# Kernel tuning notes

Measured on AMD Instinct MI355X. Metric: run time of the kernel, lower is better.

## Reference

```python
import jax, jax.numpy as jnp
import numpy as np
import math


def setup_inputs() -> dict:
    key = jax.random.key(0)
    ks = jax.random.split(key, 5)
    B, L, H = 16384, 336, 168
    T = L + H
    T_air = jax.random.normal(ks[0], (B, T), dtype=jnp.float32) * 8.0 + 10.0
    T_obs = T_air + jax.random.normal(ks[1], (B, T), dtype=jnp.float32) * 2.0
    wind = jax.random.uniform(ks[2], (B, T), dtype=jnp.float32) * 10.0
    par = jax.random.uniform(ks[3], (B, T), dtype=jnp.float32) * 500.0
    dt = jax.random.uniform(ks[4], (B, T), dtype=jnp.float32) * 3600.0 + 1800.0
    k_init = 1e-4
    k_raw = jnp.float32(k_init + math.log(-math.expm1(-k_init)))  # softplus inverse
    return {
        "T_obs": T_obs, "T_air": T_air, "wind": wind, "par": par, "dt": dt,
        "L_hist": L,
        "k_raw": k_raw,
        "log_q": jnp.float32(-8.0), "log_r": jnp.float32(-4.0),
        "log_p0": jnp.float32(-2.0), "log_q_scale": jnp.float32(0.0),
        "theta_par_lin": jnp.float32(1e-5), "theta_par_quad": jnp.float32(1e-8),
        "theta_wind_cool": jnp.float32(-1e-5), "theta_sensible": jnp.float32(-1e-6),
        "theta_forced_conv": jnp.float32(-1e-7),
    }


def reference(T_obs, T_air, wind, par, dt, L_hist, k_raw, log_q, log_r, log_p0,
              log_q_scale, theta_par_lin, theta_par_quad, theta_wind_cool,
              theta_sensible, theta_forced_conv):
    B, T_total = T_obs.shape
    L = int(L_hist)
    H = T_total - L

    k = jax.nn.softplus(k_raw)
    q = jnp.exp(log_q)
    q_scale = jnp.exp(log_q_scale)
    R = jnp.exp(log_r)
    P0 = jnp.exp(log_p0)

    def predict(T, P, Ta, w, p, dtt):
        dT = T - Ta
        cl = (theta_par_lin * p + theta_par_quad * p * p + theta_wind_cool * w
              + theta_sensible * dT + theta_forced_conv * w * dT)
        T_pred = jnp.clip(T - k * dT * dtt + cl * dtt, -50.0, 100.0)
        F = jnp.clip(1.0 - k * dtt + (theta_sensible + theta_forced_conv * w) * dtt, -2.0, 2.0)
        P_pred = jnp.clip(F * F * P + q_scale * q * dtt, 1e-10, 1e6)
        return T_pred, P_pred

    def filt_step(carry, xs):
        T, P = carry
        Ta, w, p, dtt, y = xs
        Tp, Pp = predict(T, P, Ta, w, p, dtt)
        S = Pp + R
        K = Pp / S
        T_upd = Tp + K * (y - Tp)
        P_upd = (1.0 - K) ** 2 * Pp + K * K * R
        return (T_upd, P_upd), None

    s0 = T_obs[:, 0]
    P0b = jnp.broadcast_to(P0, (B,)).astype(T_obs.dtype)

    # filtering over t = 1 .. L-1 (forcing from t-1, dt/obs at t)
    filt_xs = (T_air[:, :L - 1].T, wind[:, :L - 1].T, par[:, :L - 1].T,
               jnp.clip(dt[:, 1:L], 1.0, None).T, T_obs[:, 1:L].T)
    (s, P), _ = jax.lax.scan(filt_step, (s0, P0b), filt_xs)

    def fcst_step(carry, xs):
        T, P = carry
        Ta, w, p, dtt = xs
        Tp, Pp = predict(T, P, Ta, w, p, dtt)
        return (Tp, Pp), (Tp, Pp)

    # open-loop forecast over t = L .. L+H-1 (forcing from idx-1)
    fcst_xs = (T_air[:, L - 1:L + H - 1].T, wind[:, L - 1:L + H - 1].T,
               par[:, L - 1:L + H - 1].T, jnp.clip(dt[:, L:], 1.0, None).T)
    _, (T_preds, T_vars) = jax.lax.scan(fcst_step, (s, P), fcst_xs)

    return T_preds.T, T_vars.T  # each [B, H]
```

## Files before the change

### kernel.cpp

```cpp
#include <hip/hip_runtime.h>

namespace {
constexpr int kB = 16384;
constexpr int kL = 336;
constexpr int kH = 168;
constexpr int kT = 504;
constexpr int kW = 16;
constexpr int kNW = 32;
constexpr int kFW = 21;
constexpr int kIS = 66;
constexpr int kITile = kW * kIS;
constexpr int kOS = 17;
constexpr int kOTile = 64 * kOS;
}

__device__ inline void fwait(int* f, int target) {
    int guard = 0;
    while (__hip_atomic_load(f, __ATOMIC_RELAXED, __HIP_MEMORY_SCOPE_WORKGROUP) < target) {
        __builtin_amdgcn_s_sleep(1);
        if (++guard > (1 << 22)) break;
    }
    asm volatile("" ::: "memory");
}
__device__ inline void fpost(int* f, int lane) {
    asm volatile("s_waitcnt lgkmcnt(0)" ::: "memory");
    if (lane == 0)
        __hip_atomic_fetch_add(f, 1, __ATOMIC_RELAXED, __HIP_MEMORY_SCOPE_WORKGROUP);
}

__global__ __launch_bounds__(256, 1)
void kf_fused(const float* __restrict__ g_obs,
              const float* __restrict__ g_air,
              const float* __restrict__ g_wind,
              const float* __restrict__ g_par,
              const float* __restrict__ g_dt,
              const float* __restrict__ s_k_raw,
              const float* __restrict__ s_log_q,
              const float* __restrict__ s_log_r,
              const float* __restrict__ s_log_p0,
              const float* __restrict__ s_log_qs,
              const float* __restrict__ s_th_pl,
              const float* __restrict__ s_th_pq,
              const float* __restrict__ s_th_wc,
              const float* __restrict__ s_th_s,
              const float* __restrict__ s_th_fc,
              float* __restrict__ out)
{
    __shared__ float s_in[5][2][kITile];
    __shared__ float s_oT[2][kOTile];
    __shared__ float s_oV[2][kOTile];
    __shared__ int   s_flag[8];

    const int tid = threadIdx.x, wid = tid >> 6, lane = tid & 63;
    const int b0 = blockIdx.x * 64;

    if (tid < 8) s_flag[tid] = 0;
    __syncthreads();

    int* pcAW = &s_flag[0];
    int* pcPD = &s_flag[1];
    int* pcY  = &s_flag[2];
    int* cc   = &s_flag[3];
    int* sc   = &s_flag[4];

    const int iq = lane & 3;
    const int ir = lane >> 2;

    auto issue = [&](const float* __restrict__ g, int w, float4* r) {
        int t = w * kW + iq * 4;
        if (t > kT - 4) t = kT - 4;
#pragma unroll
        for (int i = 0; i < 4; ++i)
            r[i] = *(const float4*)(g + (size_t)(b0 + 16 * i + ir) * kT + t);
    };
    auto stash = [&](const float4* r, float* dst) {
        const int tb = iq * 4;
#pragma unroll
        for (int i = 0; i < 4; ++i) {
            const int row = 16 * i + ir;
            dst[(tb + 0) * kIS + row] = r[i].x;
            dst[(tb + 1) * kIS + row] = r[i].y;
            dst[(tb + 2) * kIS + row] = r[i].z;
            dst[(tb + 3) * kIS + row] = r[i].w;
        }
    };

    if (wid == 1 || wid == 2) {
        const float* g0 = (wid == 1) ? g_air  : g_par;
        const float* g1 = (wid == 1) ? g_wind : g_dt;
        float* base0 = (wid == 1) ? &s_in[0][0][0] : &s_in[2][0][0];
        float* base1 = (wid == 1) ? &s_in[1][0][0] : &s_in[3][0][0];
        int* pc = (wid == 1) ? pcAW : pcPD;

        float4 a0[4], b0r[4], a1[4], b1r[4];
        issue(g0, 0, a0); issue(g1, 0, b0r);
        issue(g0, 1, a1); issue(g1, 1, b1r);
        __builtin_amdgcn_sched_barrier(0);
        for (int w = 0; w < kNW; ++w) {
            if (w >= 2) fwait(cc, w - 1);
            if (w & 1) {
                stash(a1, base0 + kITile); stash(b1r, base1 + kITile);
                fpost(pc, lane);
                if (w + 2 < kNW) { issue(g0, w + 2, a1); issue(g1, w + 2, b1r); }
            } else {
                stash(a0, base0); stash(b0r, base1);
                fpost(pc, lane);
                if (w + 2 < kNW) { issue(g0, w + 2, a0); issue(g1, w + 2, b0r); }
            }
            __builtin_amdgcn_sched_barrier(0);
        }
    } else if (wid == 3) {
        float4 y0[4], y1[4];
        issue(g_obs, 0, y0); issue(g_obs, 1, y1);
        __builtin_amdgcn_sched_barrier(0);
        for (int w = 0; w < kFW; ++w) {
            if (w >= 2) fwait(cc, w - 1);
            if (w & 1) {
                stash(y1, &s_in[4][1][0]);
                fpost(pcY, lane);
                if (w + 2 < kFW) issue(g_obs, w + 2, y1);
            } else {
                stash(y0, &s_in[4][0][0]);
                fpost(pcY, lane);
                if (w + 2 < kFW) issue(g_obs, w + 2, y0);
            }
            __builtin_amdgcn_sched_barrier(0);
        }
        const int rq = lane & 3, rr = lane >> 2;
        float* outT = out;
        float* outV = out + (size_t)kB * kH;
        for (int w = kFW; w < kNW; ++w) {
            fwait(cc, w + 1);
            const int bi = w & 1;
            const int h0 = (w - kFW) * kW;
            const int nq = (w == kNW - 1) ? 2 : 4;
#pragma unroll
            for (int i = 0; i < 4; ++i) {
                const int r = 16 * i + rr;
                if (rq < nq) {
                    const float4 tv = *(const float4*)&s_oT[bi][r * kOS + rq * 4];
                    const float4 vv = *(const float4*)&s_oV[bi][r * kOS + rq * 4];
                    *(float4*)&outT[(size_t)(b0 + r) * kH + h0 + rq * 4] = tv;
                    *(float4*)&outV[(size_t)(b0 + r) * kH + h0 + rq * 4] = vv;
                }
            }
            fpost(sc, lane);
        }
    } else {
        const float kpar = log1pf(expf(s_k_raw[0]));
        const float qq   = expf(s_log_q[0]) * expf(s_log_qs[0]);
        const float R    = expf(s_log_r[0]);
        float P          = expf(s_log_p0[0]);
        const float th_pl = s_th_pl[0], th_pq = s_th_pq[0], th_wc = s_th_wc[0];
        const float th_s  = s_th_s[0],  th_fc = s_th_fc[0];
        float Tst = 0.0f, aC = 0.0f, wC = 0.0f, pC = 0.0f;

        for (int w = 0; w < kNW; ++w) {
            const int bi = w & 1;
            fwait(pcAW, w + 1);
            fwait(pcPD, w + 1);
            if (w < kFW) fwait(pcY, w + 1);
            if (w >= kFW + 2) fwait(sc, w - (kFW + 1));

            const float* A  = &s_in[0][bi][0];
            const float* Wd = &s_in[1][bi][0];
            const float* Pr = &s_in[2][bi][0];
            const float* Dd = &s_in[3][bi][0];
            const float* Yy = &s_in[4][bi][0];

            if (w < kFW) {
                int trel = 0;
                if (w == 0) {
                    Tst = Yy[lane]; aC = A[lane]; wC = Wd[lane]; pC = Pr[lane];
                    trel = 1;
                }
                for (; trel < kW; ++trel) {
                    const int ix = trel * kIS + lane;
                    const float dtt = fmaxf(Dd[ix], 1.0f);
                    const float y   = Yy[ix];
                    const float a = A[ix], wv = Wd[ix], pv = Pr[ix];
                    const float dT  = Tst - aC;
                    const float gk  = fmaf(th_fc, wC, th_s) - kpar;
                    const float base = fmaf(pC, fmaf(th_pq, pC, th_pl), th_wc * wC);
                    const float Tp = fminf(fmaxf(fmaf(fmaf(gk, dT, base), dtt, Tst), -50.0f), 100.0f);
                    const float F  = fminf(fmaxf(fmaf(gk, dtt, 1.0f), -2.0f), 2.0f);
                    const float Pp = fminf(fmaxf(fmaf(F * F, P, qq * dtt), 1e-10f), 1e6f);
                    const float Kg = Pp * __builtin_amdgcn_rcpf(Pp + R);
                    Tst = fmaf(Kg, y - Tp, Tp);
                    const float omk = 1.0f - Kg;
                    P = fmaf(omk * omk, Pp, Kg * Kg * R);
                    aC = a; wC = wv; pC = pv;
                }
            } else {
                float* oT = &s_oT[bi][lane * kOS];
                float* oV = &s_oV[bi][lane * kOS];
#pragma unroll
                for (int trel = 0; trel < kW; ++trel) {
                    const int ix = trel * kIS + lane;
                    const float dtt = fmaxf(Dd[ix], 1.0f);
                    const float a = A[ix], wv = Wd[ix], pv = Pr[ix];
                    const float dT  = Tst - aC;
                    const float gk  = fmaf(th_fc, wC, th_s) - kpar;
                    const float base = fmaf(pC, fmaf(th_pq, pC, th_pl), th_wc * wC);
                    Tst = fminf(fmaxf(fmaf(fmaf(gk, dT, base), dtt, Tst), -50.0f), 100.0f);
                    const float F = fminf(fmaxf(fmaf(gk, dtt, 1.0f), -2.0f), 2.0f);
                    P = fminf(fmaxf(fmaf(F * F, P, qq * dtt), 1e-10f), 1e6f);
                    oT[trel] = Tst;
                    oV[trel] = P;
                    aC = a; wC = wv; pC = pv;
                }
            }
            fpost(cc, lane);
        }
    }
}

extern "C" void kernel_launch(void* const* d_in, const int* in_sizes, int n_in,
                              void* d_out, int out_size, void* d_ws, size_t ws_size,
                              hipStream_t stream) {
    const float* g_obs  = (const float*)d_in[0];
    const float* g_air  = (const float*)d_in[1];
    const float* g_wind = (const float*)d_in[2];
    const float* g_par  = (const float*)d_in[3];
    const float* g_dt   = (const float*)d_in[4];
    const float* k_raw  = (const float*)d_in[6];
    const float* log_q  = (const float*)d_in[7];
    const float* log_r  = (const float*)d_in[8];
    const float* log_p0 = (const float*)d_in[9];
    const float* log_qs = (const float*)d_in[10];
    const float* th_pl  = (const float*)d_in[11];
    const float* th_pq  = (const float*)d_in[12];
    const float* th_wc  = (const float*)d_in[13];
    const float* th_s   = (const float*)d_in[14];
    const float* th_fc  = (const float*)d_in[15];
    float* out = (float*)d_out;

    dim3 grid(kB / 64), block(256);
    hipLaunchKernelGGL(kf_fused, grid, block, 0, stream,
                       g_obs, g_air, g_wind, g_par, g_dt,
                       k_raw, log_q, log_r, log_p0, log_qs,
                       th_pl, th_pq, th_wc, th_s, th_fc, out);
}
```

Measured before the change: 219.5 us.

## Switch LDS input tiles to row-major float4 layout and alias obs/output buffers

Input tiles in shared memory move from a time-major layout with scalar transposing stores to a row-major layout padded to 20 floats, written and read as float4. The compute wave now loads four timesteps per float4 with double-buffered prefetch inside a fully unrolled 4x4 step loop, so per-step scalar LDS reads are replaced by vector reads that can overlap the serial recurrence. The observation staging buffer and the output staging buffers now share one LDS region to reduce shared-memory footprint. This relies on obs staging (filter windows) and output staging (forecast windows) never being live at the same time. Risks include bank conflicts from the 20-float row stride and greater register pressure.

```diff
diff --git a/kernel.cpp b/kernel.cpp
--- a/kernel.cpp
+++ b/kernel.cpp
@@ -8,10 +8,10 @@
 constexpr int kW = 16;
 constexpr int kNW = 32;
 constexpr int kFW = 21;
-constexpr int kIS = 66;
-constexpr int kITile = kW * kIS;
+constexpr int kRS = 20;
+constexpr int kBuf = 64 * kRS;
 constexpr int kOS = 17;
-constexpr int kOTile = 64 * kOS;
+constexpr int kOv = 4352;
 }
 
 __device__ inline void fwait(int* f, int target) {
@@ -46,9 +46,8 @@
               const float* __restrict__ s_th_fc,
               float* __restrict__ out)
 {
-    __shared__ float s_in[5][2][kITile];
-    __shared__ float s_oT[2][kOTile];
-    __shared__ float s_oV[2][kOTile];
+    __shared__ float s_in[4][2][kBuf];
+    __shared__ float s_ov[kOv];
     __shared__ int   s_flag[8];
 
     const int tid = threadIdx.x, wid = tid >> 6, lane = tid & 63;
@@ -74,15 +73,9 @@
             r[i] = *(const float4*)(g + (size_t)(b0 + 16 * i + ir) * kT + t);
     };
     auto stash = [&](const float4* r, float* dst) {
-        const int tb = iq * 4;
-#pragma unroll
-        for (int i = 0; i < 4; ++i) {
-            const int row = 16 * i + ir;
-            dst[(tb + 0) * kIS + row] = r[i].x;
-            dst[(tb + 1) * kIS + row] = r[i].y;
-            dst[(tb + 2) * kIS + row] = r[i].z;
-            dst[(tb + 3) * kIS + row] = r[i].w;
-        }
+#pragma unroll
+        for (int i = 0; i < 4; ++i)
+            *(float4*)(dst + (16 * i + ir) * kRS + iq * 4) = r[i];
     };
 
     if (wid == 1 || wid == 2) {
@@ -92,20 +85,20 @@
         float* base1 = (wid == 1) ? &s_in[1][0][0] : &s_in[3][0][0];
         int* pc = (wid == 1) ? pcAW : pcPD;
 
-        float4 a0[4], b0r[4], a1[4], b1r[4];
-        issue(g0, 0, a0); issue(g1, 0, b0r);
-        issue(g0, 1, a1); issue(g1, 1, b1r);
+        float4 a0[4], c0[4], a1[4], c1[4];
+        issue(g0, 0, a0); issue(g1, 0, c0);
+        issue(g0, 1, a1); issue(g1, 1, c1);
         __builtin_amdgcn_sched_barrier(0);
         for (int w = 0; w < kNW; ++w) {
             if (w >= 2) fwait(cc, w - 1);
             if (w & 1) {
-                stash(a1, base0 + kITile); stash(b1r, base1 + kITile);
+                stash(a1, base0 + kBuf); stash(c1, base1 + kBuf);
                 fpost(pc, lane);
-                if (w + 2 < kNW) { issue(g0, w + 2, a1); issue(g1, w + 2, b1r); }
+                if (w + 2 < kNW) { issue(g0, w + 2, a1); issue(g1, w + 2, c1); }
             } else {
-                stash(a0, base0); stash(b0r, base1);
+                stash(a0, base0); stash(c0, base1);
                 fpost(pc, lane);
-                if (w + 2 < kNW) { issue(g0, w + 2, a0); issue(g1, w + 2, b0r); }
+                if (w + 2 < kNW) { issue(g0, w + 2, a0); issue(g1, w + 2, c0); }
             }
             __builtin_amdgcn_sched_barrier(0);
         }
@@ -116,11 +109,11 @@
         for (int w = 0; w < kFW; ++w) {
             if (w >= 2) fwait(cc, w - 1);
             if (w & 1) {
-                stash(y1, &s_in[4][1][0]);
+                stash(y1, &s_ov[kBuf]);
                 fpost(pcY, lane);
                 if (w + 2 < kFW) issue(g_obs, w + 2, y1);
             } else {
-                stash(y0, &s_in[4][0][0]);
+                stash(y0, &s_ov[0]);
                 fpost(pcY, lane);
                 if (w + 2 < kFW) issue(g_obs, w + 2, y0);
             }
@@ -138,8 +131,8 @@
             for (int i = 0; i < 4; ++i) {
                 const int r = 16 * i + rr;
                 if (rq < nq) {
-                    const float4 tv = *(const float4*)&s_oT[bi][r * kOS + rq * 4];
-                    const float4 vv = *(const float4*)&s_oV[bi][r * kOS + rq * 4];
+                    const float4 tv = *(const float4*)&s_ov[bi * 2176 + r * kOS + rq * 4];
+                    const float4 vv = *(const float4*)&s_ov[bi * 2176 + 1088 + r * kOS + rq * 4];
                     *(float4*)&outT[(size_t)(b0 + r) * kH + h0 + rq * 4] = tv;
                     *(float4*)&outV[(size_t)(b0 + r) * kH + h0 + rq * 4] = vv;
                 }
@@ -155,60 +148,84 @@
         const float th_s  = s_th_s[0],  th_fc = s_th_fc[0];
         float Tst = 0.0f, aC = 0.0f, wC = 0.0f, pC = 0.0f;
 
+        auto ks = [&](float ad, float wd, float pd, float D, float Y) {
+            const float dtt = fmaxf(D, 1.0f);
+            const float gk  = fmaf(th_fc, wd, th_s) - kpar;
+            const float bs  = fmaf(pd, fmaf(th_pq, pd, th_pl), th_wc * wd);
+            const float Fr  = fminf(fmaxf(fmaf(gk, dtt, 1.0f), -2.0f), 2.0f);
+            const float Pp  = fminf(fmaxf(fmaf(Fr * Fr, P, qq * dtt), 1e-10f), 1e6f);
+            const float Kg  = Pp * __builtin_amdgcn_rcpf(Pp + R);
+            const float dT  = Tst - ad;
+            const float Tp  = fminf(fmaxf(fmaf(fmaf(gk, dT, bs), dtt, Tst), -50.0f), 100.0f);
+            Tst = fmaf(Kg, Y - Tp, Tp);
+            const float omk = 1.0f - Kg;
+            P = fmaf(omk * omk, Pp, Kg * Kg * R);
+        };
+        auto fs = [&](float ad, float wd, float pd, float D) {
+            const float dtt = fmaxf(D, 1.0f);
+            const float gk  = fmaf(th_fc, wd, th_s) - kpar;
+            const float bs  = fmaf(pd, fmaf(th_pq, pd, th_pl), th_wc * wd);
+            const float Fr  = fminf(fmaxf(fmaf(gk, dtt, 1.0f), -2.0f), 2.0f);
+            P   = fminf(fmaxf(fmaf(Fr * Fr, P, qq * dtt), 1e-10f), 1e6f);
+            const float dT  = Tst - ad;
+            Tst = fminf(fmaxf(fmaf(fmaf(gk, dT, bs), dtt, Tst), -50.0f), 100.0f);
+        };
+
         for (int w = 0; w < kNW; ++w) {
             const int bi = w & 1;
             fwait(pcAW, w + 1);
             fwait(pcPD, w + 1);
-            if (w < kFW) fwait(pcY, w + 1);
+            const bool filt = w < kFW;
+            if (filt) fwait(pcY, w + 1);
             if (w >= kFW + 2) fwait(sc, w - (kFW + 1));
 
-            const float* A  = &s_in[0][bi][0];
-            const float* Wd = &s_in[1][bi][0];
-            const float* Pr = &s_in[2][bi][0];
-            const float* Dd = &s_in[3][bi][0];
-            const float* Yy = &s_in[4][bi][0];
-
-            if (w < kFW) {
-                int trel = 0;
-                if (w == 0) {
-                    Tst = Yy[lane]; aC = A[lane]; wC = Wd[lane]; pC = Pr[lane];
-                    trel = 1;
+            const float* Ab = &s_in[0][bi][lane * kRS];
+            const float* Wb = &s_in[1][bi][lane * kRS];
+            const float* Pb = &s_in[2][bi][lane * kRS];
+            const float* Db = &s_in[3][bi][lane * kRS];
+            const float* Yb = &s_ov[bi * kBuf] + lane * kRS;
+            float* oT = &s_ov[bi * 2176 + lane * kOS];
+            float* oV = &s_ov[bi * 2176 + 1088 + lane * kOS];
+
+            float4 qa[2], qw[2], qp[2], qd[2], qy[2];
+            qa[0] = *(const float4*)(Ab);
+            qw[0] = *(const float4*)(Wb);
+            qp[0] = *(const float4*)(Pb);
+            qd[0] = *(const float4*)(Db);
+            if (filt) qy[0] = *(const float4*)(Yb);
+
+#pragma unroll
+            for (int q = 0; q < 4; ++q) {
+                const int cur = q & 1, nxt = cur ^ 1;
+                if (q < 3) {
+                    qa[nxt] = *(const float4*)(Ab + 4 * (q + 1));
+                    qw[nxt] = *(const float4*)(Wb + 4 * (q + 1));
+                    qp[nxt] = *(const float4*)(Pb + 4 * (q + 1));
+                    qd[nxt] = *(const float4*)(Db + 4 * (q + 1));
+                    if (filt) qy[nxt] = *(const float4*)(Yb + 4 * (q + 1));
                 }
-                for (; trel < kW; ++trel) {
-                    const int ix = trel * kIS + lane;
-                    const float dtt = fmaxf(Dd[ix], 1.0f);
-                    const float y   = Yy[ix];
-                    const float a = A[ix], wv = Wd[ix], pv = Pr[ix];
-                    const float dT  = Tst - aC;
-                    const float gk  = fmaf(th_fc, wC, th_s) - kpar;
-                    const float base = fmaf(pC, fmaf(th_pq, pC, th_pl), th_wc * wC);
-                    const float Tp = fminf(fmaxf(fmaf(fmaf(gk, dT, base), dtt, Tst), -50.0f), 100.0f);
-                    const float F  = fminf(fmaxf(fmaf(gk, dtt, 1.0f), -2.0f), 2.0f);
-                    const float Pp = fminf(fmaxf(fmaf(F * F, P, qq * dtt), 1e-10f), 1e6f);
-                    const float Kg = Pp * __builtin_amdgcn_rcpf(Pp + R);
-                    Tst = fmaf(Kg, y - Tp, Tp);
-                    const float omk = 1.0f - Kg;
-                    P = fmaf(omk * omk, Pp, Kg * Kg * R);
-                    aC = a; wC = wv; pC = pv;
+                const float4 a = qa[cur], wv = qw[cur], pv = qp[cur],
+                             d = qd[cur], y = qy[cur];
+                if (filt) {
+                    if (w == 0 && q == 0) {
+                        Tst = y.x;
+                        ks(a.x, wv.x, pv.x, d.y, y.y);
+                        ks(a.y, wv.y, pv.y, d.z, y.z);
+                        ks(a.z, wv.z, pv.z, d.w, y.w);
+                    } else {
+                        ks(aC,  wC,   pC,   d.x, y.x);
+                        ks(a.x, wv.x, pv.x, d.y, y.y);
+                        ks(a.y, wv.y, pv.y, d.z, y.z);
+                        ks(a.z, wv.z, pv.z, d.w, y.w);
+                    }
+                } else {
+                    const int tb = q * 4;
+                    fs(aC,  wC,   pC,   d.x); oT[tb]     = Tst; oV[tb]     = P;
+                    fs(a.x, wv.x, pv.x, d.y); oT[tb + 1] = Tst; oV[tb + 1] = P;
+                    fs(a.y, wv.y, pv.y, d.z); oT[tb + 2] = Tst; oV[tb + 2] = P;
+                    fs(a.z, wv.z, pv.z, d.w); oT[tb + 3] = Tst; oV[tb + 3] = P;
                 }
-            } else {
-                float* oT = &s_oT[bi][lane * kOS];
-                float* oV = &s_oV[bi][lane * kOS];
-#pragma unroll
-                for (int trel = 0; trel < kW; ++trel) {
-                    const int ix = trel * kIS + lane;
-                    const float dtt = fmaxf(Dd[ix], 1.0f);
-                    const float a = A[ix], wv = Wd[ix], pv = Pr[ix];
-                    const float dT  = Tst - aC;
-                    const float gk  = fmaf(th_fc, wC, th_s) - kpar;
-                    const float base = fmaf(pC, fmaf(th_pq, pC, th_pl), th_wc * wC);
-                    Tst = fminf(fmaxf(fmaf(fmaf(gk, dT, base), dtt, Tst), -50.0f), 100.0f);
-                    const float F = fminf(fmaxf(fmaf(gk, dtt, 1.0f), -2.0f), 2.0f);
-                    P = fminf(fmaxf(fmaf(F * F, P, qq * dtt), 1e-10f), 1e6f);
-                    oT[trel] = Tst;
-                    oV[trel] = P;
-                    aC = a; wC = wv; pC = pv;
-                }
+                aC = a.w; wC = wv.w; pC = pv.w;
             }
             fpost(cc, lane);
         }
```

Result: slower. 245.5 us (+11.9%).
